# Kernel optimization log

Hardware: AMD Instinct MI355X
Metric: run time of the kernel (lower is better)

The kernel has to match this reference:

```python
import jax, jax.numpy as jnp
import numpy as np

N, E, IN, OUT, ED = 100000, 1600000, 64, 64, 16
NEG = -1000000000.0


def setup_inputs() -> dict:
    key = jax.random.key(0)
    ks = jax.random.split(key, 8)
    x = jax.random.normal(ks[0], (N, IN), jnp.float32)
    edge_index = jax.random.randint(ks[1], (2, E), 0, N, dtype=jnp.int32)
    edge_attr = jax.random.normal(ks[2], (E, ED), jnp.float32)
    # xavier-ish init for linear weights (stored as [in, out] for x @ W)
    Wn = jax.random.normal(ks[3], (IN, OUT), jnp.float32) * (1.0 / np.sqrt(IN))
    We = jax.random.normal(ks[4], (ED, OUT), jnp.float32) * (1.0 / np.sqrt(ED))
    att_src = jax.random.normal(ks[5], (OUT,), jnp.float32) * 0.02
    att_dst = jax.random.normal(ks[6], (OUT,), jnp.float32) * 0.02
    att_edge = jax.random.normal(ks[7], (OUT,), jnp.float32) * 0.02
    return {"x": x, "edge_index": edge_index, "edge_attr": edge_attr,
            "Wn": Wn, "We": We, "att_src": att_src, "att_dst": att_dst,
            "att_edge": att_edge}


def reference(x, edge_index, edge_attr, Wn, We, att_src, att_dst, att_edge):
    src, dst = edge_index[0], edge_index[1]
    n = x.shape[0]
    z = x @ Wn                      # [N, OUT]
    e = edge_attr @ We              # [E, OUT]
    # per-edge attention logits
    s_src = (z @ att_src)[src]      # [E]
    s_dst = (z @ att_dst)[dst]      # [E]
    s_edge = e @ att_edge           # [E]
    score = jax.nn.leaky_relu(s_src + s_dst + s_edge, negative_slope=0.2)
    # scatter softmax over dst segments (stable; matches torch amax with -1e9 init)
    max_per = jnp.maximum(jax.ops.segment_max(score, dst, num_segments=n), NEG)
    score_exp = jnp.exp(score - max_per[dst])
    denom = jax.ops.segment_sum(score_exp, dst, num_segments=n)
    alpha = score_exp / (denom[dst] + 1e-8)   # [E]
    # message + scatter-add aggregation; dropout is identity (p=0 / eval)
    msg = (z[src] + e) * alpha[:, None]       # [E, OUT]
    out = jax.ops.segment_sum(msg, dst, num_segments=n)
    # residual: in_dim == out_dim -> Identity
    return out + x
```

## Files before the change

### kernel.cpp

```cpp
#include <hip/hip_runtime.h>
#include <hip/hip_bf16.h>
#include <math.h>


__device__ __forceinline__ float bf2f(unsigned short u) {
  return __uint_as_float(((unsigned)u) << 16);
}
__device__ __forceinline__ float rdlane(float v, int k) {
  return __uint_as_float(
      (unsigned)__builtin_amdgcn_readlane((int)__float_as_uint(v), k));
}

__global__ __launch_bounds__(256) void k_init(
    const float* __restrict__ Wn, const float* __restrict__ We,
    const float* __restrict__ att_src, const float* __restrict__ att_dst,
    const float* __restrict__ att_edge, float* __restrict__ vs,
    float* __restrict__ vd, float* __restrict__ weA, int* __restrict__ total,
    int* __restrict__ count, int n) {
  int i = blockIdx.x * 256 + threadIdx.x;
  for (int j = i; j < n; j += gridDim.x * 256) count[j] = 0;
  if (blockIdx.x == 0) {
    int t = threadIdx.x;
    if (t < 64) {
      float a = 0.f, b = 0.f;
#pragma unroll
      for (int c = 0; c < 64; ++c) {
        a = fmaf(Wn[t * 64 + c], att_src[c], a);
        b = fmaf(Wn[t * 64 + c], att_dst[c], b);
      }
      vs[t] = a;
      vd[t] = b;
    } else if (t < 80) {
      float a = 0.f;
#pragma unroll
      for (int c = 0; c < 64; ++c) a = fmaf(We[(t - 64) * 64 + c], att_edge[c], a);
      weA[t - 64] = a;
    } else if (t == 80) {
      *total = 0;
    }
  }
}

__global__ __launch_bounds__(256) void k_work(
    const int* __restrict__ dst, int* __restrict__ count, int* __restrict__ pos,
    int e, const float* __restrict__ x, const float* __restrict__ Wn,
    const float* __restrict__ vs, const float* __restrict__ vd,
    unsigned short* __restrict__ zb, float* __restrict__ zs,
    float* __restrict__ zd, int n, int nbe, int nbg) {
  const int b = (int)blockIdx.x;
  if (b < nbe) {
    int i = b * 256 + threadIdx.x;
    const int stride = nbe * 256;
    for (; i < e; i += stride) pos[i] = atomicAdd(&count[dst[i]], 1);
  } else if (b < nbe + nbg) {
    const int lane = threadIdx.x & 63;
    const int wid = ((b - nbe) * 256 + threadIdx.x) >> 6;
    const int nw = nbg * 4;
    float wn[64];
#pragma unroll
    for (int k = 0; k < 64; ++k) wn[k] = Wn[k * 64 + lane];
    for (int r = wid; r < n; r += nw) {
      const int ru = __builtin_amdgcn_readfirstlane(r);
      const float* xr = x + (size_t)ru * 64;
      float a0 = 0.f, a1 = 0.f, a2 = 0.f, a3 = 0.f;
#pragma unroll
      for (int k = 0; k < 64; k += 4) {
        a0 = fmaf(xr[k], wn[k], a0);
        a1 = fmaf(xr[k + 1], wn[k + 1], a1);
        a2 = fmaf(xr[k + 2], wn[k + 2], a2);
        a3 = fmaf(xr[k + 3], wn[k + 3], a3);
      }
      float acc = (a0 + a1) + (a2 + a3);
      __hip_bfloat16 bb = __float2bfloat16(acc);
      zb[(size_t)ru * 64 + lane] = *reinterpret_cast<unsigned short*>(&bb);
    }
  } else {
    int r = (b - nbe - nbg) * 256 + threadIdx.x;
    if (r >= n) return;
    const float4* xr = (const float4*)(x + (size_t)r * 64);
    const float4* vs4 = (const float4*)vs;
    const float4* vd4 = (const float4*)vd;
    float s = 0.f, d = 0.f;
#pragma unroll
    for (int j = 0; j < 16; ++j) {
      float4 q = xr[j];
      float4 a = vs4[j], bb = vd4[j];
      s = fmaf(q.x, a.x, fmaf(q.y, a.y, fmaf(q.z, a.z, fmaf(q.w, a.w, s))));
      d = fmaf(q.x, bb.x, fmaf(q.y, bb.y, fmaf(q.z, bb.z, fmaf(q.w, bb.w, d))));
    }
    zs[r] = s;
    zd[r] = d;
  }
}

__global__ __launch_bounds__(256) void k_offsets(const int* __restrict__ count,
                                                 int* __restrict__ start,
                                                 int* __restrict__ total, int n) {
  __shared__ int sdata[256];
  __shared__ int sbase;
  const int tid = threadIdx.x;
  const int i = blockIdx.x * 256 + tid;
  int c = (i < n) ? count[i] : 0;
  int v = c;
  sdata[tid] = v;
  __syncthreads();
  for (int off = 1; off < 256; off <<= 1) {
    int t = (tid >= off) ? sdata[tid - off] : 0;
    __syncthreads();
    v += t;
    sdata[tid] = v;
    __syncthreads();
  }
  if (tid == 255) sbase = atomicAdd(total, v);
  __syncthreads();
  if (i < n) start[i] = sbase + (v - c);
}

__global__ __launch_bounds__(256) void k_scatter(
    const int* __restrict__ src, const int* __restrict__ dst,
    const int* __restrict__ pos, const float* __restrict__ zs,
    const float* __restrict__ zd, const float* __restrict__ ea,
    const float* __restrict__ weA, const int* __restrict__ start,
    uint4* __restrict__ es, int e) {
  int i = blockIdx.x * 256 + threadIdx.x;
  if (i >= e) return;
  int s = src[i], d = dst[i], p = pos[i];
  size_t slot = (size_t)start[d] + p;
  const float4* eap = (const float4*)(ea + (size_t)i * 16);
  float4 q0 = eap[0], q1 = eap[1], q2 = eap[2], q3 = eap[3];
  float sed = q0.x * weA[0] + q0.y * weA[1] + q0.z * weA[2] + q0.w * weA[3] +
              q1.x * weA[4] + q1.y * weA[5] + q1.z * weA[6] + q1.w * weA[7] +
              q2.x * weA[8] + q2.y * weA[9] + q2.z * weA[10] + q2.w * weA[11] +
              q3.x * weA[12] + q3.y * weA[13] + q3.z * weA[14] + q3.w * weA[15];
  float sv = zs[s] + zd[d] + sed;
  float sc = (sv > 0.f) ? sv : 0.2f * sv;
  es[slot] = make_uint4((unsigned)s, __float_as_uint(sc), (unsigned)i, 0u);
}

__global__ __launch_bounds__(64) void k_agg(
    const float* __restrict__ x, const unsigned short* __restrict__ zb,
    const float* __restrict__ ea, const float* __restrict__ We,
    const int* __restrict__ start, const int* __restrict__ count,
    const uint4* __restrict__ es, float* __restrict__ out, int n, int e) {
  const int lane = threadIdx.x & 63;
  const int grp = lane >> 4;
  const int gl = lane & 15;
  const int nw = gridDim.x;
  int d = blockIdx.x;
  if (d >= n) return;
  const int emax = e - 1;

  int s0 = start[d], cnt = count[d];
  int q0 = (cnt * grp) >> 2;
  int q1 = (cnt * (grp + 1)) >> 2;
  uint4 hp[4];
#pragma unroll
  for (int j = 0; j < 4; ++j) {
    int tt = min(q0 + j, q1 - 1); tt = max(tt, 0);
    hp[j] = es[min((size_t)(s0 + tt), (size_t)emax)];
  }

  while (true) {
    int dn = d + nw, sn0 = 0, cn = 0, qn0 = 0, qn1 = 0;
    uint4 hpn[4];
    const bool more = dn < n;
    if (more) {
      sn0 = start[dn];
      cn = count[dn];
      qn0 = (cn * grp) >> 2;
      qn1 = (cn * (grp + 1)) >> 2;
#pragma unroll
      for (int j = 0; j < 4; ++j) {
        int tt = min(qn0 + j, qn1 - 1); tt = max(tt, 0);
        hpn[j] = es[min((size_t)(sn0 + tt), (size_t)emax)];
      }
    }

    float dsum = 0.f, ag = 0.f;
    float4 msg = make_float4(0.f, 0.f, 0.f, 0.f);

    for (int t = q0; t < q1; t += 4) {
      uint4 h[4];
      float w[4];
      ushort4 zr[4];
      float av[4];
      if (t == q0) {
#pragma unroll
        for (int j = 0; j < 4; ++j) h[j] = hp[j];
      } else {
#pragma unroll
        for (int j = 0; j < 4; ++j) h[j] = es[(size_t)s0 + min(t + j, q1 - 1)];
      }
#pragma unroll
      for (int j = 0; j < 4; ++j) {
        zr[j] = *(const ushort4*)(zb + (size_t)h[j].x * 64 + gl * 4);
        av[j] = ea[(size_t)h[j].z * 16 + gl];
      }
#pragma unroll
      for (int j = 0; j < 4; ++j)
        w[j] = (t + j < q1) ? __expf(__uint_as_float(h[j].y)) : 0.f;
#pragma unroll
      for (int j = 0; j < 4; ++j) {
        dsum += w[j];
        msg.x = fmaf(w[j], bf2f(zr[j].x), msg.x);
        msg.y = fmaf(w[j], bf2f(zr[j].y), msg.y);
        msg.z = fmaf(w[j], bf2f(zr[j].z), msg.z);
        msg.w = fmaf(w[j], bf2f(zr[j].w), msg.w);
        ag = fmaf(w[j], av[j], ag);
      }
    }

    dsum += __shfl_xor(dsum, 16);
    dsum += __shfl_xor(dsum, 32);
    msg.x += __shfl_xor(msg.x, 16); msg.x += __shfl_xor(msg.x, 32);
    msg.y += __shfl_xor(msg.y, 16); msg.y += __shfl_xor(msg.y, 32);
    msg.z += __shfl_xor(msg.z, 16); msg.z += __shfl_xor(msg.z, 32);
    msg.w += __shfl_xor(msg.w, 16); msg.w += __shfl_xor(msg.w, 32);
    ag += __shfl_xor(ag, 16);
    ag += __shfl_xor(ag, 32);

    const float4* We4 = (const float4*)We;
    float4 evec = make_float4(0.f, 0.f, 0.f, 0.f);
#pragma unroll
    for (int k = 0; k < 16; ++k) {
      float agk = rdlane(ag, k);
      float4 wef = We4[k * 16 + gl];
      evec.x = fmaf(agk, wef.x, evec.x);
      evec.y = fmaf(agk, wef.y, evec.y);
      evec.z = fmaf(agk, wef.z, evec.z);
      evec.w = fmaf(agk, wef.w, evec.w);
    }

    if (grp == 0) {
      float inv = 1.f / (dsum + 1e-8f);
      const float4 xr = *(const float4*)(x + (size_t)d * 64 + gl * 4);
      float4 r;
      r.x = fmaf(msg.x + evec.x, inv, xr.x);
      r.y = fmaf(msg.y + evec.y, inv, xr.y);
      r.z = fmaf(msg.z + evec.z, inv, xr.z);
      r.w = fmaf(msg.w + evec.w, inv, xr.w);
      *(float4*)(out + (size_t)d * 64 + gl * 4) = r;
    }

    if (!more) break;
    d = dn; s0 = sn0; cnt = cn; q0 = qn0; q1 = qn1;
#pragma unroll
    for (int j = 0; j < 4; ++j) hp[j] = hpn[j];
  }
}

extern "C" void kernel_launch(void* const* d_in, const int* in_sizes, int n_in,
                              void* d_out, int out_size, void* d_ws, size_t ws_size,
                              hipStream_t stream) {
  const float* x = (const float*)d_in[0];
  const int* ei = (const int*)d_in[1];
  const float* ea = (const float*)d_in[2];
  const float* Wn = (const float*)d_in[3];
  const float* We = (const float*)d_in[4];
  const float* att_src = (const float*)d_in[5];
  const float* att_dst = (const float*)d_in[6];
  const float* att_edge = (const float*)d_in[7];
  float* out = (float*)d_out;

  const int N = in_sizes[0] / 64;
  const int E = in_sizes[1] / 2;
  const int* src = ei;
  const int* dst = ei + E;

  char* p = (char*)d_ws;
  auto carve = [&](size_t bytes) {
    void* q = (void*)p;
    p += (bytes + 255) & ~(size_t)255;
    return q;
  };
  unsigned short* zb = (unsigned short*)carve((size_t)N * 64 * 2);
  float* zs = (float*)carve((size_t)N * sizeof(float));
  float* zd = (float*)carve((size_t)N * sizeof(float));
  int* count = (int*)carve((size_t)N * sizeof(int));
  int* startp = (int*)carve((size_t)N * sizeof(int));
  int* pos = (int*)carve((size_t)E * sizeof(int));
  float* weA = (float*)carve(64);
  float* vs = (float*)carve(256);
  float* vd = (float*)carve(256);
  int* total = (int*)carve(64);
  uint4* es = (uint4*)carve((size_t)E * 16);

  const int nbe = 2048;
  const int nbg = 2048;
  const int nbz = (N + 255) / 256;
  k_init<<<256, 256, 0, stream>>>(Wn, We, att_src, att_dst, att_edge, vs, vd,
                                  weA, total, count, N);
  k_work<<<nbe + nbg + nbz, 256, 0, stream>>>(dst, count, pos, E, x, Wn, vs, vd,
                                              zb, zs, zd, N, nbe, nbg);
  k_offsets<<<(N + 255) / 256, 256, 0, stream>>>(count, startp, total, N);
  k_scatter<<<(E + 255) / 256, 256, 0, stream>>>(src, dst, pos, zs, zd, ea, weA,
                                                 startp, es, E);
  k_agg<<<16384, 64, 0, stream>>>(x, zb, ea, We, startp, count, es, out, N, E);
}
```

Measured before the change: 237.9 us.

## Pack edge records into 64-bit words and fold init kernel into other kernels

```diff
diff --git a/kernel.cpp b/kernel.cpp
--- a/kernel.cpp
+++ b/kernel.cpp
@@ -1,5 +1,6 @@
 #include <hip/hip_runtime.h>
 #include <hip/hip_bf16.h>
+#include <hip/hip_fp16.h>
 #include <math.h>
 
 
@@ -10,41 +11,26 @@
   return __uint_as_float(
       (unsigned)__builtin_amdgcn_readlane((int)__float_as_uint(v), k));
 }
-
-__global__ __launch_bounds__(256) void k_init(
-    const float* __restrict__ Wn, const float* __restrict__ We,
-    const float* __restrict__ att_src, const float* __restrict__ att_dst,
-    const float* __restrict__ att_edge, float* __restrict__ vs,
-    float* __restrict__ vd, float* __restrict__ weA, int* __restrict__ total,
-    int* __restrict__ count, int n) {
-  int i = blockIdx.x * 256 + threadIdx.x;
-  for (int j = i; j < n; j += gridDim.x * 256) count[j] = 0;
-  if (blockIdx.x == 0) {
-    int t = threadIdx.x;
-    if (t < 64) {
-      float a = 0.f, b = 0.f;
-#pragma unroll
-      for (int c = 0; c < 64; ++c) {
-        a = fmaf(Wn[t * 64 + c], att_src[c], a);
-        b = fmaf(Wn[t * 64 + c], att_dst[c], b);
-      }
-      vs[t] = a;
-      vd[t] = b;
-    } else if (t < 80) {
-      float a = 0.f;
-#pragma unroll
-      for (int c = 0; c < 64; ++c) a = fmaf(We[(t - 64) * 64 + c], att_edge[c], a);
-      weA[t - 64] = a;
-    } else if (t == 80) {
-      *total = 0;
-    }
-  }
+__device__ __forceinline__ unsigned long long pack_rec(unsigned s, unsigned e,
+                                                       float sc) {
+  __half h = __float2half(sc);
+  unsigned short hu = *reinterpret_cast<unsigned short*>(&h);
+  return (unsigned long long)s | ((unsigned long long)e << 17) |
+         ((unsigned long long)hu << 38);
+}
+__device__ __forceinline__ void unpack_rec(unsigned long long r, unsigned& s,
+                                           unsigned& e, float& sc) {
+  s = (unsigned)(r & 0x1FFFFull);
+  e = (unsigned)((r >> 17) & 0x1FFFFFull);
+  unsigned short hu = (unsigned short)(r >> 38);
+  __half h = *reinterpret_cast<__half*>(&hu);
+  sc = __half2float(h);
 }
 
 __global__ __launch_bounds__(256) void k_work(
     const int* __restrict__ dst, int* __restrict__ count, int* __restrict__ pos,
     int e, const float* __restrict__ x, const float* __restrict__ Wn,
-    const float* __restrict__ vs, const float* __restrict__ vd,
+    const float* __restrict__ att_src, const float* __restrict__ att_dst,
     unsigned short* __restrict__ zb, float* __restrict__ zs,
     float* __restrict__ zd, int n, int nbe, int nbg) {
   const int b = (int)blockIdx.x;
@@ -75,11 +61,25 @@
       zb[(size_t)ru * 64 + lane] = *reinterpret_cast<unsigned short*>(&bb);
     }
   } else {
-    int r = (b - nbe - nbg) * 256 + threadIdx.x;
+    __shared__ __align__(16) float svs[64];
+    __shared__ __align__(16) float svd[64];
+    const int t = threadIdx.x;
+    if (t < 64) {
+      float a = 0.f, bb = 0.f;
+#pragma unroll
+      for (int c = 0; c < 64; ++c) {
+        a = fmaf(Wn[t * 64 + c], att_src[c], a);
+        bb = fmaf(Wn[t * 64 + c], att_dst[c], bb);
+      }
+      svs[t] = a;
+      svd[t] = bb;
+    }
+    __syncthreads();
+    int r = (b - nbe - nbg) * 256 + t;
     if (r >= n) return;
     const float4* xr = (const float4*)(x + (size_t)r * 64);
-    const float4* vs4 = (const float4*)vs;
-    const float4* vd4 = (const float4*)vd;
+    const float4* vs4 = (const float4*)svs;
+    const float4* vd4 = (const float4*)svd;
     float s = 0.f, d = 0.f;
 #pragma unroll
     for (int j = 0; j < 16; ++j) {
@@ -93,9 +93,17 @@
   }
 }
 
-__global__ __launch_bounds__(256) void k_offsets(const int* __restrict__ count,
-                                                 int* __restrict__ start,
-                                                 int* __restrict__ total, int n) {
+__global__ __launch_bounds__(256) void k_offsets(
+    const int* __restrict__ count, int* __restrict__ start,
+    int* __restrict__ total, const float* __restrict__ We,
+    const float* __restrict__ att_edge, float* __restrict__ weA, int n) {
+  if (blockIdx.x == 0 && threadIdx.x >= 240) {
+    int t = threadIdx.x - 240;
+    float a = 0.f;
+#pragma unroll
+    for (int c = 0; c < 64; ++c) a = fmaf(We[t * 64 + c], att_edge[c], a);
+    weA[t] = a;
+  }
   __shared__ int sdata[256];
   __shared__ int sbase;
   const int tid = threadIdx.x;
@@ -121,7 +129,7 @@
     const int* __restrict__ pos, const float* __restrict__ zs,
     const float* __restrict__ zd, const float* __restrict__ ea,
     const float* __restrict__ weA, const int* __restrict__ start,
-    uint4* __restrict__ es, int e) {
+    unsigned long long* __restrict__ es, int e) {
   int i = blockIdx.x * 256 + threadIdx.x;
   if (i >= e) return;
   int s = src[i], d = dst[i], p = pos[i];
@@ -134,14 +142,15 @@
               q3.x * weA[12] + q3.y * weA[13] + q3.z * weA[14] + q3.w * weA[15];
   float sv = zs[s] + zd[d] + sed;
   float sc = (sv > 0.f) ? sv : 0.2f * sv;
-  es[slot] = make_uint4((unsigned)s, __float_as_uint(sc), (unsigned)i, 0u);
+  es[slot] = pack_rec((unsigned)s, (unsigned)i, sc);
 }
 
 __global__ __launch_bounds__(64) void k_agg(
     const float* __restrict__ x, const unsigned short* __restrict__ zb,
     const float* __restrict__ ea, const float* __restrict__ We,
     const int* __restrict__ start, const int* __restrict__ count,
-    const uint4* __restrict__ es, float* __restrict__ out, int n, int e) {
+    const unsigned long long* __restrict__ es, float* __restrict__ out, int n,
+    int e) {
   const int lane = threadIdx.x & 63;
   const int grp = lane >> 4;
   const int gl = lane & 15;
@@ -153,7 +162,7 @@
   int s0 = start[d], cnt = count[d];
   int q0 = (cnt * grp) >> 2;
   int q1 = (cnt * (grp + 1)) >> 2;
-  uint4 hp[4];
+  unsigned long long hp[4];
 #pragma unroll
   for (int j = 0; j < 4; ++j) {
     int tt = min(q0 + j, q1 - 1); tt = max(tt, 0);
@@ -162,7 +171,7 @@
 
   while (true) {
     int dn = d + nw, sn0 = 0, cn = 0, qn0 = 0, qn1 = 0;
-    uint4 hpn[4];
+    unsigned long long hpn[4];
     const bool more = dn < n;
     if (more) {
       sn0 = start[dn];
@@ -180,10 +189,10 @@
     float4 msg = make_float4(0.f, 0.f, 0.f, 0.f);
 
     for (int t = q0; t < q1; t += 4) {
-      uint4 h[4];
-      float w[4];
+      unsigned long long h[4];
+      unsigned sj[4], ej[4];
+      float scj[4], w[4], av[4];
       ushort4 zr[4];
-      float av[4];
       if (t == q0) {
 #pragma unroll
         for (int j = 0; j < 4; ++j) h[j] = hp[j];
@@ -192,13 +201,15 @@
         for (int j = 0; j < 4; ++j) h[j] = es[(size_t)s0 + min(t + j, q1 - 1)];
       }
 #pragma unroll
+      for (int j = 0; j < 4; ++j) unpack_rec(h[j], sj[j], ej[j], scj[j]);
+#pragma unroll
       for (int j = 0; j < 4; ++j) {
-        zr[j] = *(const ushort4*)(zb + (size_t)h[j].x * 64 + gl * 4);
-        av[j] = ea[(size_t)h[j].z * 16 + gl];
+        zr[j] = *(const ushort4*)(zb + (size_t)sj[j] * 64 + gl * 4);
+        av[j] = ea[(size_t)ej[j] * 16 + gl];
       }
 #pragma unroll
       for (int j = 0; j < 4; ++j)
-        w[j] = (t + j < q1) ? __expf(__uint_as_float(h[j].y)) : 0.f;
+        w[j] = (t + j < q1) ? __expf(scj[j]) : 0.f;
 #pragma unroll
       for (int j = 0; j < 4; ++j) {
         dsum += w[j];
@@ -276,23 +287,23 @@
   unsigned short* zb = (unsigned short*)carve((size_t)N * 64 * 2);
   float* zs = (float*)carve((size_t)N * sizeof(float));
   float* zd = (float*)carve((size_t)N * sizeof(float));
-  int* count = (int*)carve((size_t)N * sizeof(int));
+  int* count = (int*)carve((size_t)(N + 64) * sizeof(int));
   int* startp = (int*)carve((size_t)N * sizeof(int));
   int* pos = (int*)carve((size_t)E * sizeof(int));
   float* weA = (float*)carve(64);
-  float* vs = (float*)carve(256);
-  float* vd = (float*)carve(256);
-  int* total = (int*)carve(64);
-  uint4* es = (uint4*)carve((size_t)E * 16);
+  unsigned long long* es =
+      (unsigned long long*)carve((size_t)E * 8);
+  int* total = count + N;
 
   const int nbe = 2048;
   const int nbg = 2048;
   const int nbz = (N + 255) / 256;
-  k_init<<<256, 256, 0, stream>>>(Wn, We, att_src, att_dst, att_edge, vs, vd,
-                                  weA, total, count, N);
-  k_work<<<nbe + nbg + nbz, 256, 0, stream>>>(dst, count, pos, E, x, Wn, vs, vd,
-                                              zb, zs, zd, N, nbe, nbg);
-  k_offsets<<<(N + 255) / 256, 256, 0, stream>>>(count, startp, total, N);
+  (void)hipMemsetAsync(count, 0, (size_t)(N + 64) * sizeof(int), stream);
+  k_work<<<nbe + nbg + nbz, 256, 0, stream>>>(dst, count, pos, E, x, Wn,
+                                              att_src, att_dst, zb, zs, zd, N,
+                                              nbe, nbg);
+  k_offsets<<<(N + 255) / 256, 256, 0, stream>>>(count, startp, total, We,
+                                                 att_edge, weA, N);
   k_scatter<<<(E + 255) / 256, 256, 0, stream>>>(src, dst, pos, zs, zd, ea, weA,
                                                  startp, es, E);
   k_agg<<<16384, 64, 0, stream>>>(x, zb, ea, We, startp, count, es, out, N, E);
```

Result: no change. 237.3 us (-0.2%).
